# Kernel tuning notes

Measured on AMD Instinct MI355X. Metric: run time of the kernel, lower is better.

Reference implementation:

```python
import jax, jax.numpy as jnp
import numpy as np

SHOTS = 5  # kernel height of all convs; K must equal SHOTS


def _conv2d(x, w, b, stride, pad):
    # x: (N, C, H, W), w: (O, I, kh, kw)
    y = jax.lax.conv_general_dilated(
        x, w, window_strides=stride, padding=pad,
        dimension_numbers=("NCHW", "OIHW", "NCHW"))
    return y + b[None, :, None, None]


def setup_inputs() -> dict:
    key = jax.random.key(0)
    ks = jax.random.split(key, 10)
    B, N, K, D, NQ = 8, 20, SHOTS, 230, 200
    s = 0.05
    return {
        "S": jax.random.normal(ks[0], (B, N, K, D), jnp.float32),
        "Q": jax.random.normal(ks[1], (B, NQ, D), jnp.float32),
        "fc_w": jax.random.normal(ks[2], (D, D), jnp.float32) * s,
        "fc_b": jax.random.normal(ks[3], (D,), jnp.float32) * s,
        "conv1_w": jax.random.normal(ks[4], (32, 1, SHOTS, 1), jnp.float32) * s,
        "conv1_b": jax.random.normal(ks[5], (32,), jnp.float32) * s,
        "conv2_w": jax.random.normal(ks[6], (64, 32, SHOTS, 1), jnp.float32) * s,
        "conv2_b": jax.random.normal(ks[7], (64,), jnp.float32) * s,
        "convf_w": jax.random.normal(ks[8], (1, 64, SHOTS, 1), jnp.float32) * s,
        "convf_b": jax.random.normal(ks[9], (1,), jnp.float32) * s,
    }


def reference(S, Q, fc_w, fc_b, conv1_w, conv1_b, conv2_w, conv2_b, convf_w, convf_b):
    B, N, K, D = S.shape
    NQ = Q.shape[1]
    p = SHOTS // 2

    # ---- conv score extraction over the K (shot) axis ----
    x = S.reshape(B * N, 1, K, D)
    x = jax.nn.relu(_conv2d(x, conv1_w, conv1_b, (1, 1), [(p, p), (0, 0)]))
    x = jax.nn.relu(_conv2d(x, conv2_w, conv2_b, (1, 1), [(p, p), (0, 0)]))
    # dropout is identity in eval mode
    x = jax.nn.relu(_conv2d(x, convf_w, convf_b, (SHOTS, 1), [(0, 0), (0, 0)]))
    score = x.reshape(B, N, D)  # BxNxD

    # ---- hybrid attention prototype ----
    # fc applied to broadcast-expanded tensors == fc applied once, then broadcast
    Sf = S @ fc_w.T + fc_b            # B x N x K x D
    Qf = Q @ fc_w.T + fc_b            # B x NQ x D
    if K == 1:
        S_repre = jnp.broadcast_to(S.mean(-2)[:, None], (B, NQ, N, D))
    else:
        # tanh(S_fc * Q_fc).sum(-1) -> softmax over K
        t = jnp.tanh(Sf[:, None, :, :, :] * Qf[:, :, None, None, :])  # B,NQ,N,K,D
        att = jax.nn.softmax(t.sum(-1), axis=-1)                      # B,NQ,N,K
        S_repre = jnp.einsum("bqnk,bnkd->bqnd", att, S)               # B,NQ,N,D

    # ---- weighted squared L2 distance ----
    diff = S_repre - Q[:, :, None, :]                                  # B,NQ,N,D
    logits = -jnp.sum(diff * diff * score[:, None, :, :] * 700.0, axis=-1)  # B,NQ,N
    return (logits, S)
```

## Files before the change

### kernel.cpp

```cpp
#include <hip/hip_runtime.h>
#include <hip/hip_bf16.h>

typedef _Float16 f16x8 __attribute__((ext_vector_type(8)));
typedef float f32x4 __attribute__((ext_vector_type(4)));

#define BB 8
#define NN 20
#define KK 5
#define DD 230
#define NQ 200
#define QST 256

#define NB_BFC 240
#define NB_BP  200
#define NB_CP  180
#define NB_CONV 575
#define NB_FC2 38
#define NB_ATT 800

static __device__ __forceinline__ unsigned int pk2(float a, float b) {
    union { __fp16 h[2] __attribute__((aligned(4))); unsigned int u; } v;
    v.h[0] = (__fp16)a; v.h[1] = (__fp16)b; return v.u;
}

__global__ void k_pre(const float* __restrict__ fc_w,
                      const float* __restrict__ w2, const float* __restrict__ b2,
                      const float* __restrict__ wf,
                      _Float16* __restrict__ Bfc, _Float16* __restrict__ Bp,
                      float2* __restrict__ tblg,
                      const float* __restrict__ S, float* __restrict__ Scopy) {
    const int bid = blockIdx.x, tid = threadIdx.x;
    if (bid < NB_BFC) {
        int g = bid * 256 + tid;
        int kg = g & 31;
        int ncl = (g >> 5) & 15;
        int tk = g >> 9;
        int nt = tk >> 3, ks = tk & 7;
        int n = nt * 16 + ncl, k = ks * 32 + kg;
        float val = (n < DD && k < DD) ? fc_w[n * DD + k] : 0.f;
        Bfc[g] = (_Float16)val;
    } else if (bid < NB_BFC + NB_BP) {
        int g = (bid - NB_BFC) * 256 + tid;
        int kg = g & 31;
        int ncl = (g >> 5) & 15;
        int tk = g >> 9;
        int nt = tk / 5, ks = tk - nt * 5;
        int n = nt * 16 + ncl, k = ks * 32 + kg;
        int o = n / 5, i = n % 5;
        int c = k / 5, j = k - c * 5;
        int t = j - i + 2;
        float val = (t >= 0 && t < 5) ? w2[(o * 32 + c) * 5 + t] : 0.f;
        Bp[g] = (_Float16)val;
        if (g < 320) {
            int o2 = g / 5, i2 = g % 5;
            tblg[g] = make_float2(b2[o2], wf[o2 * 5 + i2]);
        }
    } else {
        int g = (bid - NB_BFC - NB_BP) * 256 + tid;
        if (g < 46000) ((float4*)Scopy)[g] = ((const float4*)S)[g];
    }
}

__global__ __launch_bounds__(512)
void k_main(const float* __restrict__ S, const float* __restrict__ Q,
            const float* __restrict__ w1, const float* __restrict__ b1,
            const _Float16* __restrict__ Bp, const _Float16* __restrict__ Bfc,
            const float2* __restrict__ tblg, float* __restrict__ sc,
            const float* __restrict__ fc_b,
            float* __restrict__ Sf, float* __restrict__ Qf) {
    __shared__ __align__(16) _Float16 XU[64 * 264];
    __shared__ float xfp[8][2][16];
    const int bid = blockIdx.x, tid = threadIdx.x;
    const int lane = tid & 63;
    const int w = __builtin_amdgcn_readfirstlane(tid >> 6);
    const int ncl = lane & 15;
    const int kg8 = (lane >> 4) * 8;
    const int g4 = lane >> 4;

    if (bid >= NB_CONV) {
        const int m0 = (bid - NB_CONV) * 64;
        for (int e = tid; e < 64 * 58; e += 512) {
            int row = e / 58, c4 = e - row * 58;
            int grow = m0 + row;
            float4 v = make_float4(0.f, 0.f, 0.f, 0.f);
            if (grow < 2400) {
                const float* inp = (grow < 800) ? S + (size_t)grow * DD
                                                : Q + (size_t)(grow - 800) * DD;
                if (c4 < 57) v = *(const float4*)&inp[c4 * 4];
                else { v.x = inp[228]; v.y = inp[229]; }
            }
            _Float16* xp = &XU[row * 264 + c4 * 4];
            xp[0] = (_Float16)v.x; xp[1] = (_Float16)v.y;
            xp[2] = (_Float16)v.z; xp[3] = (_Float16)v.w;
        }
        for (int e = tid; e < 64 * 16; e += 512) {
            int row = e >> 4, cc = 232 + (e & 15) * 2;
            *(unsigned int*)&XU[row * 264 + cc] = 0u;
        }
        __syncthreads();

        const int msub = w & 3;
        const int ngrp = w >> 2;
        f16x8 af[8];
#pragma unroll
        for (int ks = 0; ks < 8; ks++)
            af[ks] = *(const f16x8*)&XU[(msub * 16 + ncl) * 264 + ks * 32 + kg8];

        const int nt0 = ngrp * 8;
        const int ntn = ngrp ? 7 : 8;
        for (int ti = 0; ti < ntn; ti++) {
            const int nt = nt0 + ti;
            const _Float16* bp = Bfc + ((size_t)nt * 8 * 16) * 32;
            f32x4 a = {0.f, 0.f, 0.f, 0.f};
#pragma unroll
            for (int ks = 0; ks < 8; ks++) {
                f16x8 br = *(const f16x8*)&bp[(ks * 16 + ncl) * 32 + kg8];
                a = __builtin_amdgcn_mfma_f32_16x16x32_f16(af[ks], br, a, 0, 0, 0);
            }
            const int n = nt * 16 + ncl;
            const float bias = fc_b[n < DD ? n : DD - 1];
            if (n < DD) {
#pragma unroll
                for (int r = 0; r < 4; r++) {
                    int grow = m0 + msub * 16 + g4 * 4 + r;
                    if (grow < 800)
                        Sf[(size_t)grow * DD + n] = (a[r] + bias) * 2.8853900817779268f;
                    else if (grow < 2400)
                        Qf[(size_t)(grow - 800) * QST + n] = a[r] + bias;
                }
            }
        }
        return;
    }

    const int m0 = bid * 64;
    {
        const int m = m0 + lane;
        const int img = m / DD;
        const int d = m - img * DD;
        const float* sp = S + (size_t)img * KK * DD + d;
        float in5[5];
#pragma unroll
        for (int j = 0; j < 5; j++) in5[j] = sp[j * DD];
#pragma unroll
        for (int cc = 0; cc < 4; cc++) {
            int c = w * 4 + cc;
            float wl[5];
#pragma unroll
            for (int t = 0; t < 5; t++) wl[t] = w1[c * 5 + t];
            float bb = b1[c];
#pragma unroll
            for (int i = 0; i < 5; i++) {
                float a = bb;
#pragma unroll
                for (int t = 0; t < 5; t++) {
                    int j = i + t - 2;
                    if (j >= 0 && j < 5) a = fmaf(wl[t], in5[j], a);
                }
                XU[lane * 168 + c * 5 + i] = (_Float16)fmaxf(a, 0.f);
            }
        }
    }
    __syncthreads();

    const int mh = w & 1;
    const int gq = w >> 1;
    f16x8 af0[5], af1[5];
#pragma unroll
    for (int ks = 0; ks < 5; ks++) {
        af0[ks] = *(const f16x8*)&XU[((mh * 2 + 0) * 16 + ncl) * 168 + ks * 32 + kg8];
        af1[ks] = *(const f16x8*)&XU[((mh * 2 + 1) * 16 + ncl) * 168 + ks * 32 + kg8];
    }

    float xf0 = 0.f, xf1 = 0.f;
#pragma unroll
    for (int t5 = 0; t5 < 5; t5++) {
        const int nt = gq * 5 + t5;
        const _Float16* bp = Bp + ((size_t)nt * 5 * 16) * 32;
        f16x8 br[5];
#pragma unroll
        for (int ks = 0; ks < 5; ks++)
            br[ks] = *(const f16x8*)&bp[(ks * 16 + ncl) * 32 + kg8];
        f32x4 a0 = {0.f, 0.f, 0.f, 0.f}, a1 = {0.f, 0.f, 0.f, 0.f};
#pragma unroll
        for (int ks = 0; ks < 5; ks++) {
            a0 = __builtin_amdgcn_mfma_f32_16x16x32_f16(br[ks], af0[ks], a0, 0, 0, 0);
            a1 = __builtin_amdgcn_mfma_f32_16x16x32_f16(br[ks], af1[ks], a1, 0, 0, 0);
        }
        float2 tb[4];
#pragma unroll
        for (int r = 0; r < 4; r++) tb[r] = tblg[nt * 16 + g4 * 4 + r];
#pragma unroll
        for (int r = 0; r < 4; r++) {
            xf0 = fmaf(fmaxf(a0[r] + tb[r].x, 0.f), tb[r].y, xf0);
            xf1 = fmaf(fmaxf(a1[r] + tb[r].x, 0.f), tb[r].y, xf1);
        }
    }
    xf0 += __shfl_xor(xf0, 16, 64); xf0 += __shfl_xor(xf0, 32, 64);
    xf1 += __shfl_xor(xf1, 16, 64); xf1 += __shfl_xor(xf1, 32, 64);
    if (lane < 16) { xfp[w][0][lane] = xf0; xfp[w][1][lane] = xf1; }
    __syncthreads();
    if (tid < 64) {
        const int strip = tid >> 4, col = tid & 15;
        const int mhh = strip >> 1, idx = strip & 1;
        float s = xfp[mhh][idx][col] + xfp[mhh + 2][idx][col]
                + xfp[mhh + 4][idx][col] + xfp[mhh + 6][idx][col];
        sc[m0 + strip * 16 + col] = s;
    }
}

__global__ __launch_bounds__(512)
void k_att(const float* __restrict__ Sf, const float* __restrict__ Qf,
           const float* __restrict__ S, const float* __restrict__ Q,
           const float* __restrict__ sc, const float* __restrict__ convf_b,
           float* __restrict__ out) {
    __shared__ __align__(16) _Float16 SfT[32 * 264];
    __shared__ __align__(16) float Lw[8][32];
    __shared__ __align__(16) float Qs[8][256];
    const int phys = blockIdx.x, tid = threadIdx.x;
    const int bid = (phys & 7) * 100 + (phys >> 3);
    const int lane = tid & 63;
    const int w = __builtin_amdgcn_readfirstlane(tid >> 6);
    const int b = bid / 100;
    const int nq = (bid / 25) & 3;
    const int qg = bid % 25;
    const int q = qg * 8 + w;
    const int n0 = nq * 5;
    const int ncl = lane & 15;
    const int g4 = lane >> 4;
    const int kg8 = g4 * 8;
    const float LOG2E = 1.4426950408889634f;
    const float bf0 = convf_b[0];

    const float* sfb = Sf + (size_t)(b * 100 + n0 * 5) * DD;
    for (int e = tid; e < 32 * 132; e += 512) {
        int row = e / 132, c2 = e - row * 132;
        unsigned int u = 0u;
        if (row < 25 && c2 <= 114) {
            float2 v = *(const float2*)&sfb[row * DD + 2 * c2];
            u = pk2(v.x, v.y);
        }
        *(unsigned int*)&SfT[row * 264 + 2 * c2] = u;
    }
    for (int e = tid; e < 8 * 256; e += 512) {
        int row = e >> 8, col = e & 255;
        float v = 0.f;
        if (col < DD) v = Qf[(size_t)(b * NQ + qg * 8 + row) * QST + col];
        Qs[row][col] = v;
    }
    __syncthreads();

    f16x8 ones;
#pragma unroll
    for (int j = 0; j < 8; j++) ones[j] = (_Float16)1.f;
    f32x4 acc0 = {0.f, 0.f, 0.f, 0.f}, acc1 = {0.f, 0.f, 0.f, 0.f};

    for (int ks = 0; ks < 8; ks++) {
        f32x4 qa = *(const f32x4*)&Qs[w][ks * 32 + kg8];
        f32x4 qb = *(const f32x4*)&Qs[w][ks * 32 + kg8 + 4];
        float qv[8];
#pragma unroll
        for (int j = 0; j < 4; j++) { qv[j] = qa[j]; qv[4 + j] = qb[j]; }
#pragma unroll
        for (int t = 0; t < 2; t++) {
            f16x8 s8 = *(const f16x8*)&SfT[(t * 16 + ncl) * 264 + ks * 32 + kg8];
            f16x8 vf;
#pragma unroll
            for (int j = 0; j < 8; j++) {
                float x = (float)s8[j] * qv[j];
                float e = __builtin_amdgcn_exp2f(x);
                float v = 1.f - 2.f * __builtin_amdgcn_rcpf(e + 1.f);
                vf[j] = (_Float16)v;
            }
            if (t == 0) acc0 = __builtin_amdgcn_mfma_f32_16x16x32_f16(vf, ones, acc0, 0, 0, 0);
            else        acc1 = __builtin_amdgcn_mfma_f32_16x16x32_f16(vf, ones, acc1, 0, 0, 0);
        }
    }
    if (ncl == 0) {
        *(f32x4*)&Lw[w][g4 * 4] = acc0;
        *(f32x4*)&Lw[w][16 + g4 * 4] = acc1;
    }

    int dcl[4];
    float msk[4];
#pragma unroll
    for (int i = 0; i < 4; i++) {
        int d = lane + 64 * i;
        dcl[i] = d < DD ? d : DD - 1;
        msk[i] = d < DD ? 1.f : 0.f;
    }
    float qr[4];
    const float* qp = Q + (size_t)(b * NQ + q) * DD;
#pragma unroll
    for (int i = 0; i < 4; i++) qr[i] = qp[dcl[i]];

#pragma unroll
    for (int nl = 0; nl < 5; nl++) {
        const float* lp = &Lw[w][nl * 5];
        float v0 = lp[0], v1 = lp[1], v2 = lp[2], v3 = lp[3], v4 = lp[4];
        float m = fmaxf(fmaxf(fmaxf(v0, v1), fmaxf(v2, v3)), v4);
        float e0 = __builtin_amdgcn_exp2f((v0 - m) * LOG2E);
        float e1 = __builtin_amdgcn_exp2f((v1 - m) * LOG2E);
        float e2 = __builtin_amdgcn_exp2f((v2 - m) * LOG2E);
        float e3 = __builtin_amdgcn_exp2f((v3 - m) * LOG2E);
        float e4 = __builtin_amdgcn_exp2f((v4 - m) * LOG2E);
        float inv = __builtin_amdgcn_rcpf(e0 + e1 + e2 + e3 + e4);
        float a0 = e0 * inv, a1 = e1 * inv, a2 = e2 * inv, a3 = e3 * inv, a4 = e4 * inv;
        const int n = n0 + nl;
        const float* spn = S + (size_t)(b * NN + n) * KK * DD;
        const float* s0 = sc + (size_t)(b * NN + n) * DD;
        float acc2 = 0.f;
#pragma unroll
        for (int i = 0; i < 4; i++) {
            int d = dcl[i];
            float rep = a0 * spn[d] + a1 * spn[DD + d] + a2 * spn[2 * DD + d]
                      + a3 * spn[3 * DD + d] + a4 * spn[4 * DD + d];
            float df = rep - qr[i];
            float scw = fmaxf(s0[d] + bf0, 0.f) * 700.f * msk[i];
            acc2 = fmaf(df * df, scw, acc2);
        }
#pragma unroll
        for (int off = 32; off > 0; off >>= 1) acc2 += __shfl_xor(acc2, off, 64);
        if (lane == 0) out[((size_t)b * NQ + q) * NN + n] = -acc2;
    }
}

extern "C" void kernel_launch(void* const* d_in, const int* in_sizes, int n_in,
                              void* d_out, int out_size, void* d_ws, size_t ws_size,
                              hipStream_t stream) {
    const float* S       = (const float*)d_in[0];
    const float* Q       = (const float*)d_in[1];
    const float* fc_w    = (const float*)d_in[2];
    const float* fc_b    = (const float*)d_in[3];
    const float* conv1_w = (const float*)d_in[4];
    const float* conv1_b = (const float*)d_in[5];
    const float* conv2_w = (const float*)d_in[6];
    const float* conv2_b = (const float*)d_in[7];
    const float* convf_w = (const float*)d_in[8];
    const float* convf_b = (const float*)d_in[9];
    float* out = (float*)d_out;

    float* ws = (float*)d_ws;
    float* Sf  = ws;
    float* Qf  = Sf + 184000;
    float* sc  = Qf + 409600;
    _Float16* Bp  = (_Float16*)(sc + 36800);
    _Float16* Bfc = Bp + 51200;
    float2* tblg  = (float2*)(Bfc + 61440);

    k_pre<<<NB_BFC + NB_BP + NB_CP, 256, 0, stream>>>(
        fc_w, conv2_w, conv2_b, convf_w, Bfc, Bp, tblg,
        S, out + (size_t)BB * NQ * NN);
    k_main<<<NB_CONV + NB_FC2, 512, 0, stream>>>(
        S, Q, conv1_w, conv1_b, Bp, Bfc, tblg, sc, fc_b, Sf, Qf);
    k_att<<<NB_ATT, 512, 0, stream>>>(
        Sf, Qf, S, Q, sc, convf_b, out);
}
```

Before: 61.94 us.

## Fuse weight pre-packing into main kernel and drop the pre-pass launch

Removes the k_pre kernel that packed fc_w and the banded conv2 weights into fp16 MFMA-ready layouts. k_main now builds those B fragments on the fly from the fp32 weights in global memory, and the S copy to the output moves into extra blocks of k_main. This saves one kernel launch and a global-memory round trip for the packed weights. In exchange, every block repeats the weight gathering, does scattered per-element loads with div5 index math for the banded conv matrix, and converts to fp16 in registers inside the MFMA loop.

```diff
diff --git a/kernel.cpp b/kernel.cpp
--- a/kernel.cpp
+++ b/kernel.cpp
@@ -11,63 +11,27 @@
 #define NQ 200
 #define QST 256
 
-#define NB_BFC 240
-#define NB_BP  200
-#define NB_CP  180
 #define NB_CONV 575
 #define NB_FC2 38
+#define NB_CP  90
 #define NB_ATT 800
 
 static __device__ __forceinline__ unsigned int pk2(float a, float b) {
     union { __fp16 h[2] __attribute__((aligned(4))); unsigned int u; } v;
     v.h[0] = (__fp16)a; v.h[1] = (__fp16)b; return v.u;
 }
-
-__global__ void k_pre(const float* __restrict__ fc_w,
-                      const float* __restrict__ w2, const float* __restrict__ b2,
-                      const float* __restrict__ wf,
-                      _Float16* __restrict__ Bfc, _Float16* __restrict__ Bp,
-                      float2* __restrict__ tblg,
-                      const float* __restrict__ S, float* __restrict__ Scopy) {
-    const int bid = blockIdx.x, tid = threadIdx.x;
-    if (bid < NB_BFC) {
-        int g = bid * 256 + tid;
-        int kg = g & 31;
-        int ncl = (g >> 5) & 15;
-        int tk = g >> 9;
-        int nt = tk >> 3, ks = tk & 7;
-        int n = nt * 16 + ncl, k = ks * 32 + kg;
-        float val = (n < DD && k < DD) ? fc_w[n * DD + k] : 0.f;
-        Bfc[g] = (_Float16)val;
-    } else if (bid < NB_BFC + NB_BP) {
-        int g = (bid - NB_BFC) * 256 + tid;
-        int kg = g & 31;
-        int ncl = (g >> 5) & 15;
-        int tk = g >> 9;
-        int nt = tk / 5, ks = tk - nt * 5;
-        int n = nt * 16 + ncl, k = ks * 32 + kg;
-        int o = n / 5, i = n % 5;
-        int c = k / 5, j = k - c * 5;
-        int t = j - i + 2;
-        float val = (t >= 0 && t < 5) ? w2[(o * 32 + c) * 5 + t] : 0.f;
-        Bp[g] = (_Float16)val;
-        if (g < 320) {
-            int o2 = g / 5, i2 = g % 5;
-            tblg[g] = make_float2(b2[o2], wf[o2 * 5 + i2]);
-        }
-    } else {
-        int g = (bid - NB_BFC - NB_BP) * 256 + tid;
-        if (g < 46000) ((float4*)Scopy)[g] = ((const float4*)S)[g];
-    }
+static __device__ __forceinline__ int div5(int n) {
+    return (n * 6554) >> 15;
 }
 
 __global__ __launch_bounds__(512)
 void k_main(const float* __restrict__ S, const float* __restrict__ Q,
             const float* __restrict__ w1, const float* __restrict__ b1,
-            const _Float16* __restrict__ Bp, const _Float16* __restrict__ Bfc,
-            const float2* __restrict__ tblg, float* __restrict__ sc,
-            const float* __restrict__ fc_b,
-            float* __restrict__ Sf, float* __restrict__ Qf) {
+            const float* __restrict__ w2, const float* __restrict__ b2,
+            const float* __restrict__ wf, const float* __restrict__ fc_w,
+            const float* __restrict__ fc_b, float* __restrict__ sc,
+            float* __restrict__ Sf, float* __restrict__ Qf,
+            float* __restrict__ Scopy) {
     __shared__ __align__(16) _Float16 XU[64 * 264];
     __shared__ float xfp[8][2][16];
     const int bid = blockIdx.x, tid = threadIdx.x;
@@ -76,6 +40,12 @@
     const int ncl = lane & 15;
     const int kg8 = (lane >> 4) * 8;
     const int g4 = lane >> 4;
+
+    if (bid >= NB_CONV + NB_FC2) {
+        int g = (bid - NB_CONV - NB_FC2) * 512 + tid;
+        if (g < 46000) ((float4*)Scopy)[g] = ((const float4*)S)[g];
+        return;
+    }
 
     if (bid >= NB_CONV) {
         const int m0 = (bid - NB_CONV) * 64;
@@ -101,32 +71,50 @@
 
         const int msub = w & 3;
         const int ngrp = w >> 2;
+        const int abase = (msub * 16 + ncl) * 264;
         f16x8 af[8];
 #pragma unroll
         for (int ks = 0; ks < 8; ks++)
-            af[ks] = *(const f16x8*)&XU[(msub * 16 + ncl) * 264 + ks * 32 + kg8];
+            af[ks] = *(const f16x8*)&XU[abase + ks * 32 + kg8];
 
         const int nt0 = ngrp * 8;
         const int ntn = ngrp ? 7 : 8;
         for (int ti = 0; ti < ntn; ti++) {
             const int nt = nt0 + ti;
-            const _Float16* bp = Bfc + ((size_t)nt * 8 * 16) * 32;
+            const int n_f = nt * 16 + ncl;
+            const float vmn = (n_f < DD) ? 1.f : 0.f;
+            const float* fw = fc_w + (size_t)(n_f < DD ? n_f : 0) * DD;
             f32x4 a = {0.f, 0.f, 0.f, 0.f};
 #pragma unroll
             for (int ks = 0; ks < 8; ks++) {
-                f16x8 br = *(const f16x8*)&bp[(ks * 16 + ncl) * 32 + kg8];
+                const int k0 = ks * 32 + kg8;
+                f16x8 br;
+                if (ks < 7) {
+#pragma unroll
+                    for (int t2 = 0; t2 < 4; t2++) {
+                        float2 p = *(const float2*)&fw[k0 + 2 * t2];
+                        br[2 * t2]     = (_Float16)(p.x * vmn);
+                        br[2 * t2 + 1] = (_Float16)(p.y * vmn);
+                    }
+                } else {
+#pragma unroll
+                    for (int j = 0; j < 8; j++) {
+                        int k = k0 + j;
+                        float v = fw[k < DD ? k : DD - 1];
+                        br[j] = (_Float16)((k < DD) ? v * vmn : 0.f);
+                    }
+                }
                 a = __builtin_amdgcn_mfma_f32_16x16x32_f16(af[ks], br, a, 0, 0, 0);
             }
-            const int n = nt * 16 + ncl;
-            const float bias = fc_b[n < DD ? n : DD - 1];
-            if (n < DD) {
+            const float bias = fc_b[n_f < DD ? n_f : DD - 1];
+            if (n_f < DD) {
 #pragma unroll
                 for (int r = 0; r < 4; r++) {
                     int grow = m0 + msub * 16 + g4 * 4 + r;
                     if (grow < 800)
-                        Sf[(size_t)grow * DD + n] = (a[r] + bias) * 2.8853900817779268f;
+                        Sf[(size_t)grow * DD + n_f] = (a[r] + bias) * 2.8853900817779268f;
                     else if (grow < 2400)
-                        Qf[(size_t)(grow - 800) * QST + n] = a[r] + bias;
+                        Qf[(size_t)(grow - 800) * QST + n_f] = a[r] + bias;
                 }
             }
         }
@@ -176,24 +164,44 @@
 #pragma unroll
     for (int t5 = 0; t5 < 5; t5++) {
         const int nt = gq * 5 + t5;
-        const _Float16* bp = Bp + ((size_t)nt * 5 * 16) * 32;
+        const int n_l = nt * 16 + ncl;
+        const int o_l = div5(n_l);
+        const int i_l = n_l - o_l * 5;
+        const int basew = o_l * 160 + 2 - i_l;
         f16x8 br[5];
 #pragma unroll
-        for (int ks = 0; ks < 5; ks++)
-            br[ks] = *(const f16x8*)&bp[(ks * 16 + ncl) * 32 + kg8];
+        for (int ks = 0; ks < 5; ks++) {
+            const int k0 = ks * 32 + kg8;
+            const int m0w = k0 - 5 * div5(k0);
+            f16x8 fr;
+#pragma unroll
+            for (int j = 0; j < 8; j++) {
+                int m = m0w + j;
+                m -= (m >= 5) ? 5 : 0;
+                m -= (m >= 5) ? 5 : 0;
+                bool valid = (unsigned)(m - i_l + 2) < 5u;
+                int addr = basew + k0 + j;
+                addr = addr < 0 ? 0 : (addr > 10239 ? 10239 : addr);
+                float v = w2[addr];
+                fr[j] = (_Float16)(valid ? v : 0.f);
+            }
+            br[ks] = fr;
+        }
         f32x4 a0 = {0.f, 0.f, 0.f, 0.f}, a1 = {0.f, 0.f, 0.f, 0.f};
 #pragma unroll
         for (int ks = 0; ks < 5; ks++) {
             a0 = __builtin_amdgcn_mfma_f32_16x16x32_f16(br[ks], af0[ks], a0, 0, 0, 0);
             a1 = __builtin_amdgcn_mfma_f32_16x16x32_f16(br[ks], af1[ks], a1, 0, 0, 0);
         }
-        float2 tb[4];
-#pragma unroll
-        for (int r = 0; r < 4; r++) tb[r] = tblg[nt * 16 + g4 * 4 + r];
 #pragma unroll
         for (int r = 0; r < 4; r++) {
-            xf0 = fmaf(fmaxf(a0[r] + tb[r].x, 0.f), tb[r].y, xf0);
-            xf1 = fmaf(fmaxf(a1[r] + tb[r].x, 0.f), tb[r].y, xf1);
+            int n_r = nt * 16 + g4 * 4 + r;
+            int o_r = div5(n_r);
+            int i_r = n_r - o_r * 5;
+            float tbx = b2[o_r];
+            float tby = wf[o_r * 5 + i_r];
+            xf0 = fmaf(fmaxf(a0[r] + tbx, 0.f), tby, xf0);
+            xf1 = fmaf(fmaxf(a1[r] + tbx, 0.f), tby, xf1);
         }
     }
     xf0 += __shfl_xor(xf0, 16, 64); xf0 += __shfl_xor(xf0, 32, 64);
@@ -344,15 +352,10 @@
     float* Sf  = ws;
     float* Qf  = Sf + 184000;
     float* sc  = Qf + 409600;
-    _Float16* Bp  = (_Float16*)(sc + 36800);
-    _Float16* Bfc = Bp + 51200;
-    float2* tblg  = (float2*)(Bfc + 61440);
-
-    k_pre<<<NB_BFC + NB_BP + NB_CP, 256, 0, stream>>>(
-        fc_w, conv2_w, conv2_b, convf_w, Bfc, Bp, tblg,
-        S, out + (size_t)BB * NQ * NN);
-    k_main<<<NB_CONV + NB_FC2, 512, 0, stream>>>(
-        S, Q, conv1_w, conv1_b, Bp, Bfc, tblg, sc, fc_b, Sf, Qf);
+
+    k_main<<<NB_CONV + NB_FC2 + NB_CP, 512, 0, stream>>>(
+        S, Q, conv1_w, conv1_b, conv2_w, conv2_b, convf_w, fc_w, fc_b,
+        sc, Sf, Qf, out + (size_t)BB * NQ * NN);
     k_att<<<NB_ATT, 512, 0, stream>>>(
         Sf, Qf, S, Q, sc, convf_b, out);
 }
```

Measured after the change: 107.0 us. 1.73x slower.
